# Performance work log

Hardware: AMD Instinct MI355X
Metric: run time of the kernel (lower is better)

## Reference

```python
import jax, jax.numpy as jnp
import numpy as np

H = 1024
NH = 16
HD = H // NH  # 64

def setup_inputs() -> dict:
    key = jax.random.key(0)
    ks = jax.random.split(key, 6)
    B, S = 2, 2048
    hidden_states = jax.random.normal(ks[0], (B, S, H), dtype=jnp.float32)
    attention_mask = jnp.ones((B, S), dtype=jnp.int32)
    sc = 1.0 / np.sqrt(H)
    Wq = jax.random.normal(ks[1], (H, H), dtype=jnp.float32) * sc
    Wk = jax.random.normal(ks[2], (H, H), dtype=jnp.float32) * sc
    Wv = jax.random.normal(ks[3], (H, H), dtype=jnp.float32) * sc
    Wo = jax.random.normal(ks[4], (H, H), dtype=jnp.float32) * sc
    return {"hidden_states": hidden_states, "attention_mask": attention_mask,
            "Wq": Wq, "Wk": Wk, "Wv": Wv, "Wo": Wo}

def reference(hidden_states, attention_mask, Wq, Wk, Wv, Wo):
    B, S, _ = hidden_states.shape
    # nn.Linear(bias=False): y = x @ W.T
    q = hidden_states @ Wq.T
    k = hidden_states @ Wk.T
    v = hidden_states @ Wv.T
    # [B, NH, S, HD]
    q = q.reshape(B, S, NH, HD).transpose(0, 2, 1, 3)
    k = k.reshape(B, S, NH, HD).transpose(0, 2, 1, 3)
    v = v.reshape(B, S, NH, HD).transpose(0, 2, 1, 3)
    # ELU+1 feature map
    q = jax.nn.elu(q) + 1.0
    k = jax.nn.elu(k) + 1.0
    # [B, NH, S, S]
    attn = jnp.einsum('bhqd,bhkd->bhqk', q, k)
    mask = attention_mask[:, None, None, :]  # [B,1,1,S]
    attn = jnp.where(mask == 0, -jnp.inf, attn)
    attn = jax.nn.softmax(attn, axis=-1)
    # dropout p=0.0 (eval) -> identity
    out = jnp.einsum('bhqk,bhkd->bhqd', attn, v)
    out = out.transpose(0, 2, 1, 3).reshape(B, S, H)
    return out @ Wo.T
```

## Files before the change

### kernel.cpp

```cpp
#include <hip/hip_runtime.h>

#define H_ 1024
#define NH_ 16
#define HD_ 64
#define B_ 2
#define S_ 2048
#define BS_ 4096

typedef _Float16 half8 __attribute__((ext_vector_type(8)));
typedef _Float16 half4_t __attribute__((ext_vector_type(4)));
typedef float floatx4 __attribute__((ext_vector_type(4)));

#define LOG2E 1.44269504088896f

__device__ __forceinline__ void async_copy16(void* lds, const void* g) {
  __builtin_amdgcn_global_load_lds(
      (const __attribute__((address_space(1))) unsigned int*)g,
      (__attribute__((address_space(3))) unsigned int*)lds, 16, 0, 0);
}

__global__ __launch_bounds__(256) void cvt_all(
    const float* __restrict__ hs, const float* __restrict__ wq,
    const float* __restrict__ wk, const float* __restrict__ wv,
    const float* __restrict__ wo,
    _Float16* __restrict__ hs_h, _Float16* __restrict__ w_h) {
  int i = blockIdx.x * 256 + threadIdx.x;
  int idx = i * 4;
  const float* src; _Float16* dst; int off;
  if (idx < BS_ * H_) {
    src = hs; dst = hs_h; off = idx;
  } else {
    int j = idx - BS_ * H_;
    int w = j >> 20;
    off = j & ((1 << 20) - 1);
    src = (w == 0) ? wq : (w == 1) ? wk : (w == 2) ? wv : wo;
    dst = w_h + (size_t)w * (H_ * H_);
  }
  float4 f = *(const float4*)(src + off);
  half4_t o;
  o.x = (_Float16)f.x; o.y = (_Float16)f.y;
  o.z = (_Float16)f.z; o.w = (_Float16)f.w;
  *(half4_t*)(dst + off) = o;
}

__global__ __launch_bounds__(256) void qkv_gemm(
    const _Float16* __restrict__ A, const _Float16* __restrict__ Wall,
    _Float16* __restrict__ qh, _Float16* __restrict__ kh,
    _Float16* __restrict__ vt) {
  const int z = blockIdx.z;
  const _Float16* W = Wall + (size_t)z * (H_ * H_);
  const int rbase = blockIdx.y * 128;
  const int cbase = blockIdx.x * 128;
  __shared__ _Float16 As[128 * 32];
  __shared__ _Float16 Bs[128 * 32];
  const int tid = threadIdx.x, lane = tid & 63, w = tid >> 6;
  const int quad = lane >> 4, l16 = lane & 15;
  const int wr = (w >> 1) * 64, wc = (w & 1) * 64;

  floatx4 zero = {0.f, 0.f, 0.f, 0.f};
  floatx4 acc[4][4];
#pragma unroll
  for (int i = 0; i < 4; ++i)
#pragma unroll
    for (int j = 0; j < 4; ++j) acc[i][j] = zero;

  const int srow = w * 32 + (lane >> 2);
  const int sseg = (lane & 3) * 8;
  const _Float16* Ag = A + (size_t)(rbase + srow) * H_ + sseg;
  const _Float16* Bg = W + (size_t)(cbase + srow) * H_ + sseg;

  for (int k0 = 0; k0 < H_; k0 += 32) {
    async_copy16(&As[(w * 32) * 32], Ag + k0);
    async_copy16(&As[(w * 32 + 16) * 32], Ag + 16 * H_ + k0);
    async_copy16(&Bs[(w * 32) * 32], Bg + k0);
    async_copy16(&Bs[(w * 32 + 16) * 32], Bg + 16 * H_ + k0);
    __syncthreads();
    half8 af[4], bf[4];
#pragma unroll
    for (int t = 0; t < 4; ++t)
      af[t] = *(half8*)&As[(wr + t * 16 + l16) * 32 + quad * 8];
#pragma unroll
    for (int t = 0; t < 4; ++t)
      bf[t] = *(half8*)&Bs[(wc + t * 16 + l16) * 32 + quad * 8];
#pragma unroll
    for (int i = 0; i < 4; ++i)
#pragma unroll
      for (int j = 0; j < 4; ++j)
        acc[i][j] = __builtin_amdgcn_mfma_f32_16x16x32_f16(af[i], bf[j],
                                                           acc[i][j], 0, 0, 0);
    __syncthreads();
  }
#pragma unroll
  for (int i = 0; i < 4; ++i) {
    int r0 = rbase + wr + i * 16 + quad * 4;
    int b = r0 >> 11, sl0 = r0 & (S_ - 1);
#pragma unroll
    for (int j = 0; j < 4; ++j) {
      int col = cbase + wc + j * 16 + l16;
      int h = col >> 6, d = col & 63;
      if (z == 2) {
        half4_t pk;
#pragma unroll
        for (int r = 0; r < 4; ++r) pk[r] = (_Float16)acc[i][j][r];
        *(half4_t*)&vt[((size_t)(b * NH_ + h) * HD_ + d) * S_ + sl0] = pk;
      } else {
        _Float16* outp = (z == 0) ? qh : kh;
        float scale = (z == 0) ? LOG2E : 1.0f;
#pragma unroll
        for (int r = 0; r < 4; ++r) {
          float x = acc[i][j][r];
          x = ((x > 0.f) ? (x + 1.f) : __expf(x)) * scale;
          outp[((size_t)(b * NH_ + h) * S_ + sl0 + r) * HD_ + d] = (_Float16)x;
        }
      }
    }
  }
}

__global__ __launch_bounds__(256, 2) void flash_attn(
    const _Float16* __restrict__ qh, const _Float16* __restrict__ kh,
    const _Float16* __restrict__ vt, const int* __restrict__ mask,
    _Float16* __restrict__ attn_out) {
  const int bh = blockIdx.y, b = bh >> 4, h = bh & 15;
  const int qbase = blockIdx.x * 128;
  const int tid = threadIdx.x, w = tid >> 6, lane = tid & 63;
  const int quad = lane >> 4, l16 = lane & 15;

  __shared__ _Float16 Kt[2][128 * 64];
  __shared__ _Float16 Vt[2][64 * 128];

  const _Float16* Q = qh + (size_t)bh * (S_ * HD_);
  const _Float16* K = kh + (size_t)bh * (S_ * HD_);
  const _Float16* Vg = vt + (size_t)bh * (HD_ * S_);
  const int* Mb = mask + b * S_;

  half8 qf[2][2];
#pragma unroll
  for (int g = 0; g < 2; ++g) {
    int qr = qbase + w * 32 + g * 16 + l16;
    qf[g][0] = *(const half8*)&Q[qr * 64 + quad * 8];
    qf[g][1] = *(const half8*)&Q[qr * 64 + 32 + quad * 8];
  }

  floatx4 zero = {0.f, 0.f, 0.f, 0.f};
  floatx4 o[2][4];
#pragma unroll
  for (int g = 0; g < 2; ++g)
#pragma unroll
    for (int i = 0; i < 4; ++i) o[g][i] = zero;
  float mi[2] = {-3e38f, -3e38f}, li[2] = {0.f, 0.f};

  const int krow_off = lane >> 3;
  const int kslot = lane & 7;
  const int kchunk = kslot ^ (krow_off & 7);
  const int vrow_off = lane >> 4;
  const int vslot = lane & 15;

  {
#pragma unroll
    for (int u = 0; u < 4; ++u) {
      int kl = w * 32 + u * 8;
      async_copy16(&Kt[0][kl * 64], K + (size_t)(kl + krow_off) * 64 + kchunk * 8);
    }
#pragma unroll
    for (int u = 0; u < 4; ++u) {
      int d0 = w * 16 + u * 4 + vrow_off;
      int c0 = vslot ^ (d0 & 15);
      async_copy16(&Vt[0][(w * 16 + u * 4) * 128], Vg + (size_t)d0 * S_ + c0 * 8);
    }
  }

  for (int kt = 0; kt < S_ / 128; ++kt) {
    const int key0 = kt * 128;
    const int buf = kt & 1;
    __syncthreads();
    if (kt < S_ / 128 - 1) {
      const int key1 = key0 + 128;
#pragma unroll
      for (int u = 0; u < 4; ++u) {
        int kl = w * 32 + u * 8;
        async_copy16(&Kt[buf ^ 1][kl * 64],
                     K + (size_t)(key1 + kl + krow_off) * 64 + kchunk * 8);
      }
#pragma unroll
      for (int u = 0; u < 4; ++u) {
        int d0 = w * 16 + u * 4 + vrow_off;
        int c0 = vslot ^ (d0 & 15);
        async_copy16(&Vt[buf ^ 1][(w * 16 + u * 4) * 128],
                     Vg + (size_t)d0 * S_ + key1 + c0 * 8);
      }
    }
    int m0 = Mb[key0 + lane];
    int m1 = Mb[key0 + 64 + lane];

    const _Float16* Kb = &Kt[buf][0];
    const _Float16* Vb = &Vt[buf][0];

    floatx4 sa[2][8];
#pragma unroll
    for (int g = 0; g < 2; ++g)
#pragma unroll
      for (int ct = 0; ct < 8; ++ct) sa[g][ct] = zero;
    {
      int s0 = quad ^ (l16 & 7);
      int s1 = (4 + quad) ^ (l16 & 7);
#pragma unroll
      for (int ct = 0; ct < 8; ++ct) {
        int key = ct * 16 + l16;
        half8 bf0 = *(half8*)&Kb[key * 64 + s0 * 8];
        half8 bf1 = *(half8*)&Kb[key * 64 + s1 * 8];
        sa[0][ct] = __builtin_amdgcn_mfma_f32_16x16x32_f16(bf0, qf[0][0], sa[0][ct], 0, 0, 0);
        sa[0][ct] = __builtin_amdgcn_mfma_f32_16x16x32_f16(bf1, qf[0][1], sa[0][ct], 0, 0, 0);
        sa[1][ct] = __builtin_amdgcn_mfma_f32_16x16x32_f16(bf0, qf[1][0], sa[1][ct], 0, 0, 0);
        sa[1][ct] = __builtin_amdgcn_mfma_f32_16x16x32_f16(bf1, qf[1][1], sa[1][ct], 0, 0, 0);
      }
    }
    if (__any((m0 == 0) || (m1 == 0))) {
#pragma unroll
      for (int ct = 0; ct < 8; ++ct)
#pragma unroll
        for (int r = 0; r < 4; ++r)
          if (Mb[key0 + ct * 16 + quad * 4 + r] == 0) {
            sa[0][ct][r] = -1e30f;
            sa[1][ct][r] = -1e30f;
          }
    }
#pragma unroll
    for (int g = 0; g < 2; ++g) {
      float mx = sa[g][0][0];
#pragma unroll
      for (int ct = 0; ct < 8; ++ct)
#pragma unroll
        for (int r = 0; r < 4; ++r) mx = fmaxf(mx, sa[g][ct][r]);
      mx = fmaxf(mx, __shfl_xor(mx, 16));
      mx = fmaxf(mx, __shfl_xor(mx, 32));
      float mn = fmaxf(mi[g], mx);
      float alpha = __builtin_amdgcn_exp2f(mi[g] - mn);
      mi[g] = mn;
      float rs = 0.f;
#pragma unroll
      for (int ct = 0; ct < 8; ++ct)
#pragma unroll
        for (int r = 0; r < 4; ++r) {
          float p = __builtin_amdgcn_exp2f(sa[g][ct][r] - mn);
          sa[g][ct][r] = p;
          rs += p;
        }
      rs += __shfl_xor(rs, 16);
      rs += __shfl_xor(rs, 32);
      li[g] = li[g] * alpha + rs;
#pragma unroll
      for (int ct2 = 0; ct2 < 4; ++ct2) {
        o[g][ct2][0] *= alpha; o[g][ct2][1] *= alpha;
        o[g][ct2][2] *= alpha; o[g][ct2][3] *= alpha;
      }
    }
#pragma unroll
    for (int ct = 0; ct < 8; ++ct) {
      half4_t p0, p1;
#pragma unroll
      for (int r = 0; r < 4; ++r) {
        p0[r] = (_Float16)sa[0][ct][r];
        p1[r] = (_Float16)sa[1][ct][r];
      }
      int chunk = (2 * ct + (quad >> 1)) ^ l16;
      int off = chunk * 8 + (quad & 1) * 4;
#pragma unroll
      for (int ct2 = 0; ct2 < 4; ++ct2) {
        int d = ct2 * 16 + l16;
        half4_t vf = *(half4_t*)&Vb[d * 128 + off];
        o[0][ct2] = __builtin_amdgcn_mfma_f32_16x16x16f16(vf, p0, o[0][ct2], 0, 0, 0);
        o[1][ct2] = __builtin_amdgcn_mfma_f32_16x16x16f16(vf, p1, o[1][ct2], 0, 0, 0);
      }
    }
  }
#pragma unroll
  for (int g = 0; g < 2; ++g) {
    float inv = 1.0f / li[g];
    int row = qbase + w * 32 + g * 16 + l16;
#pragma unroll
    for (int ct2 = 0; ct2 < 4; ++ct2) {
      half4_t pk;
#pragma unroll
      for (int r = 0; r < 4; ++r) pk[r] = (_Float16)(o[g][ct2][r] * inv);
      int d = ct2 * 16 + quad * 4;
      *(half4_t*)&attn_out[((size_t)(b * S_ + row)) * H_ + h * HD_ + d] = pk;
    }
  }
}

__global__ __launch_bounds__(256) void out_gemm(
    const _Float16* __restrict__ A, const _Float16* __restrict__ W,
    float* __restrict__ out) {
  const int rbase = blockIdx.y * 128;
  const int cbase = blockIdx.x * 64;
  __shared__ _Float16 As[128 * 32];
  __shared__ _Float16 Bs[64 * 32];
  const int tid = threadIdx.x, lane = tid & 63, w = tid >> 6;
  const int quad = lane >> 4, l16 = lane & 15;

  floatx4 zero = {0.f, 0.f, 0.f, 0.f};
  floatx4 acc[2][4];
#pragma unroll
  for (int i = 0; i < 2; ++i)
#pragma unroll
    for (int j = 0; j < 4; ++j) acc[i][j] = zero;

  const int srowA = w * 32 + (lane >> 2);
  const int srowB = w * 16 + (lane >> 2);
  const int sseg = (lane & 3) * 8;
  const _Float16* Ag = A + (size_t)(rbase + srowA) * H_ + sseg;
  const _Float16* Bg = W + (size_t)(cbase + srowB) * H_ + sseg;

  for (int k0 = 0; k0 < H_; k0 += 32) {
    async_copy16(&As[(w * 32) * 32], Ag + k0);
    async_copy16(&As[(w * 32 + 16) * 32], Ag + 16 * H_ + k0);
    async_copy16(&Bs[(w * 16) * 32], Bg + k0);
    __syncthreads();
    half8 af[2], bf[4];
#pragma unroll
    for (int t = 0; t < 2; ++t)
      af[t] = *(half8*)&As[(w * 32 + t * 16 + l16) * 32 + quad * 8];
#pragma unroll
    for (int t = 0; t < 4; ++t)
      bf[t] = *(half8*)&Bs[(t * 16 + l16) * 32 + quad * 8];
#pragma unroll
    for (int i = 0; i < 2; ++i)
#pragma unroll
      for (int j = 0; j < 4; ++j)
        acc[i][j] = __builtin_amdgcn_mfma_f32_16x16x32_f16(af[i], bf[j],
                                                           acc[i][j], 0, 0, 0);
    __syncthreads();
  }
#pragma unroll
  for (int i = 0; i < 2; ++i) {
    int r0 = rbase + w * 32 + i * 16 + quad * 4;
#pragma unroll
    for (int j = 0; j < 4; ++j) {
      int col = cbase + j * 16 + l16;
#pragma unroll
      for (int r = 0; r < 4; ++r)
        out[(size_t)(r0 + r) * H_ + col] = acc[i][j][r];
    }
  }
}

extern "C" void kernel_launch(void* const* d_in, const int* in_sizes, int n_in,
                              void* d_out, int out_size, void* d_ws,
                              size_t ws_size, hipStream_t stream) {
  const float* hs = (const float*)d_in[0];
  const int* mask = (const int*)d_in[1];
  const float* Wq = (const float*)d_in[2];
  const float* Wk = (const float*)d_in[3];
  const float* Wv = (const float*)d_in[4];
  const float* Wo = (const float*)d_in[5];
  float* out = (float*)d_out;

  _Float16* p = (_Float16*)d_ws;
  _Float16* hs_h = p; p += (size_t)BS_ * H_;
  _Float16* w_h = p;  p += (size_t)4 * H_ * H_;
  _Float16* q_h = p;  p += (size_t)BS_ * H_;
  _Float16* k_h = p;  p += (size_t)BS_ * H_;
  _Float16* v_t = p;  p += (size_t)BS_ * H_;
  _Float16* ao_h = p; p += (size_t)BS_ * H_;

  cvt_all<<<8192, 256, 0, stream>>>(hs, Wq, Wk, Wv, Wo, hs_h, w_h);
  qkv_gemm<<<dim3(8, 32, 3), 256, 0, stream>>>(hs_h, w_h, q_h, k_h, v_t);
  flash_attn<<<dim3(16, 32), 256, 0, stream>>>(q_h, k_h, v_t, mask, ao_h);
  out_gemm<<<dim3(16, 32), 256, 0, stream>>>(ao_h, w_h + (size_t)3 * H_ * H_, out);
}
```

Before: 193.1 us.

## Triple-buffer async LDS loads with XOR swizzle in QKV and output GEMMs

```diff
diff --git a/kernel.cpp b/kernel.cpp
--- a/kernel.cpp
+++ b/kernel.cpp
@@ -43,7 +43,7 @@
   *(half4_t*)(dst + off) = o;
 }
 
-__global__ __launch_bounds__(256) void qkv_gemm(
+__global__ __launch_bounds__(256, 3) void qkv_gemm(
     const _Float16* __restrict__ A, const _Float16* __restrict__ Wall,
     _Float16* __restrict__ qh, _Float16* __restrict__ kh,
     _Float16* __restrict__ vt) {
@@ -51,8 +51,8 @@
   const _Float16* W = Wall + (size_t)z * (H_ * H_);
   const int rbase = blockIdx.y * 128;
   const int cbase = blockIdx.x * 128;
-  __shared__ _Float16 As[128 * 32];
-  __shared__ _Float16 Bs[128 * 32];
+  __shared__ _Float16 Ab[3][128 * 32];
+  __shared__ _Float16 Bb[3][128 * 32];
   const int tid = threadIdx.x, lane = tid & 63, w = tid >> 6;
   const int quad = lane >> 4, l16 = lane & 15;
   const int wr = (w >> 1) * 64, wc = (w & 1) * 64;
@@ -64,32 +64,68 @@
 #pragma unroll
     for (int j = 0; j < 4; ++j) acc[i][j] = zero;
 
-  const int srow = w * 32 + (lane >> 2);
-  const int sseg = (lane & 3) * 8;
-  const _Float16* Ag = A + (size_t)(rbase + srow) * H_ + sseg;
-  const _Float16* Bg = W + (size_t)(cbase + srow) * H_ + sseg;
-
-  for (int k0 = 0; k0 < H_; k0 += 32) {
-    async_copy16(&As[(w * 32) * 32], Ag + k0);
-    async_copy16(&As[(w * 32 + 16) * 32], Ag + 16 * H_ + k0);
-    async_copy16(&Bs[(w * 32) * 32], Bg + k0);
-    async_copy16(&Bs[(w * 32 + 16) * 32], Bg + 16 * H_ + k0);
-    __syncthreads();
+  const int srow = tid >> 2;
+  const int pslot = tid & 3;
+  const int sslot = pslot ^ ((srow >> 1) & 3);
+  const _Float16* Ag = A + (size_t)(rbase + srow) * H_ + sslot * 8;
+  const _Float16* Bg = W + (size_t)(cbase + srow) * H_ + sslot * 8;
+
+  auto STAGE = [&](int s, int t) {
+    const int k0 = t * 32;
+    _Float16* ab = &Ab[s][tid * 8];
+    _Float16* bb = &Bb[s][tid * 8];
+    async_copy16(ab, Ag + k0);
+    async_copy16(ab + 2048, Ag + (size_t)64 * H_ + k0);
+    async_copy16(bb, Bg + k0);
+    async_copy16(bb + 2048, Bg + (size_t)64 * H_ + k0);
+  };
+
+  const int rsw = (l16 >> 1) & 3;
+  auto COMPUTE = [&](int s) {
+    const _Float16* Ap = &Ab[s][0];
+    const _Float16* Bp = &Bb[s][0];
     half8 af[4], bf[4];
 #pragma unroll
     for (int t = 0; t < 4; ++t)
-      af[t] = *(half8*)&As[(wr + t * 16 + l16) * 32 + quad * 8];
+      af[t] = *(const half8*)&Ap[(wr + t * 16 + l16) * 32 + (quad ^ rsw) * 8];
 #pragma unroll
     for (int t = 0; t < 4; ++t)
-      bf[t] = *(half8*)&Bs[(wc + t * 16 + l16) * 32 + quad * 8];
+      bf[t] = *(const half8*)&Bp[(wc + t * 16 + l16) * 32 + (quad ^ rsw) * 8];
+    __builtin_amdgcn_s_setprio(1);
 #pragma unroll
     for (int i = 0; i < 4; ++i)
 #pragma unroll
       for (int j = 0; j < 4; ++j)
         acc[i][j] = __builtin_amdgcn_mfma_f32_16x16x32_f16(af[i], bf[j],
                                                            acc[i][j], 0, 0, 0);
-    __syncthreads();
-  }
+    __builtin_amdgcn_s_setprio(0);
+  };
+
+  STAGE(0, 0);
+  STAGE(1, 1);
+  int sc = 0;
+  for (int t = 0; t < 30; ++t) {
+    asm volatile("s_waitcnt vmcnt(4)" ::: "memory");
+    __builtin_amdgcn_sched_barrier(0);
+    __builtin_amdgcn_s_barrier();
+    __builtin_amdgcn_sched_barrier(0);
+    int ss = sc + 2; if (ss >= 3) ss -= 3;
+    STAGE(ss, t + 2);
+    COMPUTE(sc);
+    sc = (sc == 2) ? 0 : sc + 1;
+  }
+  asm volatile("s_waitcnt vmcnt(4)" ::: "memory");
+  __builtin_amdgcn_sched_barrier(0);
+  __builtin_amdgcn_s_barrier();
+  __builtin_amdgcn_sched_barrier(0);
+  COMPUTE(sc);
+  sc = (sc == 2) ? 0 : sc + 1;
+  asm volatile("s_waitcnt vmcnt(0)" ::: "memory");
+  __builtin_amdgcn_sched_barrier(0);
+  __builtin_amdgcn_s_barrier();
+  __builtin_amdgcn_sched_barrier(0);
+  COMPUTE(sc);
+
 #pragma unroll
   for (int i = 0; i < 4; ++i) {
     int r0 = rbase + wr + i * 16 + quad * 4;
@@ -289,13 +325,13 @@
   }
 }
 
-__global__ __launch_bounds__(256) void out_gemm(
+__global__ __launch_bounds__(256, 2) void out_gemm(
     const _Float16* __restrict__ A, const _Float16* __restrict__ W,
     float* __restrict__ out) {
   const int rbase = blockIdx.y * 128;
   const int cbase = blockIdx.x * 64;
-  __shared__ _Float16 As[128 * 32];
-  __shared__ _Float16 Bs[64 * 32];
+  __shared__ _Float16 Ab[3][128 * 32];
+  __shared__ _Float16 Bb[3][64 * 32];
   const int tid = threadIdx.x, lane = tid & 63, w = tid >> 6;
   const int quad = lane >> 4, l16 = lane & 15;
 
@@ -306,32 +342,66 @@
 #pragma unroll
     for (int j = 0; j < 4; ++j) acc[i][j] = zero;
 
-  const int srowA = w * 32 + (lane >> 2);
-  const int srowB = w * 16 + (lane >> 2);
-  const int sseg = (lane & 3) * 8;
-  const _Float16* Ag = A + (size_t)(rbase + srowA) * H_ + sseg;
-  const _Float16* Bg = W + (size_t)(cbase + srowB) * H_ + sseg;
-
-  for (int k0 = 0; k0 < H_; k0 += 32) {
-    async_copy16(&As[(w * 32) * 32], Ag + k0);
-    async_copy16(&As[(w * 32 + 16) * 32], Ag + 16 * H_ + k0);
-    async_copy16(&Bs[(w * 16) * 32], Bg + k0);
-    __syncthreads();
+  const int srow = tid >> 2;
+  const int pslot = tid & 3;
+  const int sslot = pslot ^ ((srow >> 1) & 3);
+  const _Float16* Ag = A + (size_t)(rbase + srow) * H_ + sslot * 8;
+  const _Float16* Bg = W + (size_t)(cbase + srow) * H_ + sslot * 8;
+
+  auto STAGE = [&](int s, int t) {
+    const int k0 = t * 32;
+    _Float16* ab = &Ab[s][tid * 8];
+    async_copy16(ab, Ag + k0);
+    async_copy16(ab + 2048, Ag + (size_t)64 * H_ + k0);
+    async_copy16(&Bb[s][tid * 8], Bg + k0);
+  };
+
+  const int rsw = (l16 >> 1) & 3;
+  auto COMPUTE = [&](int s) {
+    const _Float16* Ap = &Ab[s][0];
+    const _Float16* Bp = &Bb[s][0];
     half8 af[2], bf[4];
 #pragma unroll
     for (int t = 0; t < 2; ++t)
-      af[t] = *(half8*)&As[(w * 32 + t * 16 + l16) * 32 + quad * 8];
+      af[t] = *(const half8*)&Ap[(w * 32 + t * 16 + l16) * 32 + (quad ^ rsw) * 8];
 #pragma unroll
     for (int t = 0; t < 4; ++t)
-      bf[t] = *(half8*)&Bs[(t * 16 + l16) * 32 + quad * 8];
+      bf[t] = *(const half8*)&Bp[(t * 16 + l16) * 32 + (quad ^ rsw) * 8];
+    __builtin_amdgcn_s_setprio(1);
 #pragma unroll
     for (int i = 0; i < 2; ++i)
 #pragma unroll
       for (int j = 0; j < 4; ++j)
         acc[i][j] = __builtin_amdgcn_mfma_f32_16x16x32_f16(af[i], bf[j],
                                                            acc[i][j], 0, 0, 0);
-    __syncthreads();
-  }
+    __builtin_amdgcn_s_setprio(0);
+  };
+
+  STAGE(0, 0);
+  STAGE(1, 1);
+  int sc = 0;
+  for (int t = 0; t < 30; ++t) {
+    asm volatile("s_waitcnt vmcnt(3)" ::: "memory");
+    __builtin_amdgcn_sched_barrier(0);
+    __builtin_amdgcn_s_barrier();
+    __builtin_amdgcn_sched_barrier(0);
+    int ss = sc + 2; if (ss >= 3) ss -= 3;
+    STAGE(ss, t + 2);
+    COMPUTE(sc);
+    sc = (sc == 2) ? 0 : sc + 1;
+  }
+  asm volatile("s_waitcnt vmcnt(3)" ::: "memory");
+  __builtin_amdgcn_sched_barrier(0);
+  __builtin_amdgcn_s_barrier();
+  __builtin_amdgcn_sched_barrier(0);
+  COMPUTE(sc);
+  sc = (sc == 2) ? 0 : sc + 1;
+  asm volatile("s_waitcnt vmcnt(0)" ::: "memory");
+  __builtin_amdgcn_sched_barrier(0);
+  __builtin_amdgcn_s_barrier();
+  __builtin_amdgcn_sched_barrier(0);
+  COMPUTE(sc);
+
 #pragma unroll
   for (int i = 0; i < 2; ++i) {
     int r0 = rbase + w * 32 + i * 16 + quad * 4;
```

After: 192.6 us. Within noise of the previous version (-0.3%).
